# Kernel tuning notes

Measured on AMD Instinct MI355X. Metric: run time of the kernel, lower is better.

Reference implementation:

```python
import jax, jax.numpy as jnp
import numpy as np

N = 500000      # examples = M * (nr+1)
K = 20          # context set size (indices[:, 3:])
NR = 24         # negatives per positive
H = 128         # hidden_channels == node feature dim
NODES = 10000   # ingredient vocabulary


def setup_inputs() -> dict:
    key = jax.random.key(0)
    ks = jax.random.split(key, 6)
    indices = jax.random.randint(ks[0], (N, 3 + K), 0, NODES)
    x = jax.random.normal(ks[1], (NODES, H), dtype=jnp.float32)
    scale = 0.02
    W1 = jax.random.normal(ks[2], (H, 3 * H), dtype=jnp.float32) * scale
    b1 = jnp.zeros((H,), jnp.float32)
    W2 = jax.random.normal(ks[3], (H // 2, H), dtype=jnp.float32) * scale
    b2 = jnp.zeros((H // 2,), jnp.float32)
    W3 = jax.random.normal(ks[4], (1, H // 2), dtype=jnp.float32) * scale
    b3 = jnp.zeros((1,), jnp.float32)
    return {"indices": indices, "nr": NR, "x": x,
            "W1": W1, "b1": b1, "W2": W2, "b2": b2, "W3": W3, "b3": b3}


def _embed_context(ctx_idx, x, nr):
    # ctx_idx: [N, K]; one context row per group of (nr+1) examples
    new_idx = ctx_idx[:-1:nr + 1]                 # [M, K]
    emb = x[new_idx]                               # [M, K, H] gather
    s = emb.sum(axis=1)                            # [M, H]
    norm = jnp.maximum((new_idx > 0).sum(axis=1), 1).astype(x.dtype)[:, None]
    mean = s / norm                                # masked mean over context
    return jnp.repeat(mean, nr + 1, axis=0)        # broadcast back to [N, H]


def reference(indices, nr, x, W1, b1, W2, b2, W3, b3):
    ing1 = x[indices[:, 0]]                        # [N, H]
    ing2 = x[indices[:, 1]]                        # [N, H]
    set_emb = _embed_context(indices[:, 3:], x, nr)  # [N, H]
    y = jnp.concatenate([ing1, ing2, set_emb], axis=1)  # [N, 3H]
    y = jax.nn.relu(y @ W1.T + b1)
    y = jax.nn.relu(y @ W2.T + b2)
    return y @ W3.T + b3                           # [N, 1]
```

## Files before the change

kernel.cpp:

```cpp
#include <hip/hip_runtime.h>
#include <hip/hip_bf16.h>

#define N_ROWS   500000
#define NR1      25
#define NGROUPS  20000
#define KCTX     20
#define H        128
#define NODES    10000
#define IDX_COLS 23

typedef __attribute__((ext_vector_type(8))) short short8;
typedef __attribute__((ext_vector_type(4))) float f32x4;

__device__ __forceinline__ unsigned pkbf(float lo, float hi) {
  __hip_bfloat162 h = __float22bfloat162_rn(make_float2(lo, hi));
  union { __hip_bfloat162 h; unsigned u; } c; c.h = h;
  return c.u;
}
__device__ __forceinline__ float lo2f(unsigned u) {
  union { unsigned u; float f; } c; c.u = u << 16; return c.f;
}
__device__ __forceinline__ float hi2f(unsigned u) {
  union { unsigned u; float f; } c; c.u = u & 0xffff0000u; return c.f;
}

#define PN 64
#define PBLK      ((NODES + PN - 1) / PN)
#define B_PG_END  ((NGROUPS + 63) / 64)
#define B_P12     B_PG_END
#define B_IDXP    (B_P12 + 4 * PBLK)
#define B_W2FP    (B_IDXP + PBLK)
#define PRE_BLOCKS (B_W2FP + 1)

__global__ __launch_bounds__(256) void k_pre(
    const int* __restrict__ indices, const float* __restrict__ x,
    const float* __restrict__ W1, const float* __restrict__ b1,
    const float* __restrict__ W2,
    unsigned short* __restrict__ Pb, unsigned short* __restrict__ Pgb,
    unsigned short* __restrict__ w2f, int2* __restrict__ idx2) {
  __shared__ __align__(16) short lds_all[24576];

  const int tid = threadIdx.x;
  const int bid = blockIdx.x;
  const int lane = tid & 63;
  const int wvid = tid >> 6;
  const int col  = lane & 15;
  const int quad = lane >> 4;

  if (bid >= B_IDXP) {
    if (bid == B_W2FP) {
#pragma unroll
      for (int i = 0; i < 4; ++i) {
        const int fi = i * 4 + wvid;
        const int kt = fi >> 2, ct = fi & 3;
        const float* __restrict__ src =
            W2 + (size_t)(ct * 16 + col) * H + kt * 32 + quad * 8;
        const float4 v0 = *(const float4*)src;
        const float4 v1 = *(const float4*)(src + 4);
        union { short8 v; unsigned u[4]; } pk;
        pk.u[0] = pkbf(v0.x, v0.y);
        pk.u[1] = pkbf(v0.z, v0.w);
        pk.u[2] = pkbf(v1.x, v1.y);
        pk.u[3] = pkbf(v1.z, v1.w);
        *(short8*)(w2f + (size_t)(fi * 64 + lane) * 8) = pk.v;
      }
    } else {
      const int stride = PBLK * 256;
      for (int r = (bid - B_IDXP) * 256 + tid; r < N_ROWS; r += stride)
        idx2[r] = make_int2(indices[(size_t)r * IDX_COLS + 0],
                            indices[(size_t)r * IDX_COLS + 1]);
    }
    return;
  }

  if (bid < B_PG_END) {
    short* w13  = lds_all;
    short* mlds = lds_all + 16384;
    const int gbase = bid * 64;

#pragma unroll
    for (int it = 0; it < 16; ++it) {
      const int f  = it * 256 + tid;
      const int j  = f >> 5;
      const int q4 = f & 31;
      const float4 v = *(const float4*)(W1 + (size_t)j * (3 * H) + 2 * H + q4 * 4);
      const int sidx = j * 128 + (((q4 >> 1) ^ (j & 7)) << 3) + (q4 & 1) * 4;
      *(unsigned*)&w13[sidx]     = pkbf(v.x, v.y);
      *(unsigned*)&w13[sidx + 2] = pkbf(v.z, v.w);
    }

    const int jj = lane * 2;
#pragma unroll
    for (int it = 0; it < 8; ++it) {
      const int ga = gbase + wvid * 16 + it;
      const int gb = ga + 8;
      const int gac = (ga < NGROUPS) ? ga : (NGROUPS - 1);
      const int gbc = (gb < NGROUPS) ? gb : (NGROUPS - 1);
      const int* __restrict__ ra = indices + (size_t)gac * NR1 * IDX_COLS + 3;
      const int* __restrict__ rb = indices + (size_t)gbc * NR1 * IDX_COLS + 3;
      float a0 = 0.f, a1 = 0.f, c0 = 0.f, c1 = 0.f;
      int ca = 0, cb = 0;
#pragma unroll
      for (int c = 0; c < KCTX; ++c) {
        const int ia = ra[c], ib = rb[c];
        const float2 va = *(const float2*)(x + (size_t)ia * H + jj);
        const float2 vb = *(const float2*)(x + (size_t)ib * H + jj);
        a0 += va.x; a1 += va.y; c0 += vb.x; c1 += vb.y;
        ca += (ia > 0) ? 1 : 0; cb += (ib > 0) ? 1 : 0;
      }
      const float rna = 1.f / (float)((ca > 1) ? ca : 1);
      const float rnb = 1.f / (float)((cb > 1) ? cb : 1);
      {
        const int row = wvid * 16 + it;
        const int sb = row * 128 + (((lane >> 2) ^ (row & 7)) << 3) + (lane & 3) * 2;
        *(unsigned*)&mlds[sb] = pkbf(a0 * rna, a1 * rna);
      }
      {
        const int row = wvid * 16 + it + 8;
        const int sb = row * 128 + (((lane >> 2) ^ (row & 7)) << 3) + (lane & 3) * 2;
        *(unsigned*)&mlds[sb] = pkbf(c0 * rnb, c1 * rnb);
      }
    }
    __syncthreads();

    short8 Af[4];
    const int arow = wvid * 16 + col;
#pragma unroll
    for (int kt = 0; kt < 4; ++kt)
      Af[kt] = *(const short8*)
          &mlds[arow * 128 + (((kt * 4 + quad) ^ (arow & 7)) << 3)];

    f32x4 acc[8];
#pragma unroll
    for (int ct = 0; ct < 8; ++ct) acc[ct] = (f32x4)(0.f);
#pragma unroll
    for (int kt = 0; kt < 4; ++kt) {
#pragma unroll
      for (int ct = 0; ct < 8; ++ct) {
        const int brow = ct * 16 + col;
        const short8 Bf = *(const short8*)
            &w13[brow * 128 + (((kt * 4 + quad) ^ (brow & 7)) << 3)];
        acc[ct] = __builtin_amdgcn_mfma_f32_16x16x32_bf16(Af[kt], Bf, acc[ct], 0, 0, 0);
      }
    }
    float b1v[8];
#pragma unroll
    for (int ct = 0; ct < 8; ++ct) b1v[ct] = b1[ct * 16 + col];
#pragma unroll
    for (int reg = 0; reg < 4; ++reg) {
      const int g2 = gbase + wvid * 16 + quad * 4 + reg;
      if (g2 < NGROUPS) {
#pragma unroll
        for (int ct = 0; ct < 8; ++ct) {
          union { unsigned u; unsigned short s[2]; } c;
          c.u = pkbf(acc[ct][reg] + b1v[ct], 0.f);
          Pgb[(size_t)g2 * H + ct * 16 + col] = c.s[0];
        }
      }
    }
    return;
  }

  {
    short* wlds = lds_all;
    const int local = bid - B_P12;
    const int m   = local / (2 * PBLK);
    const int sub = local - m * (2 * PBLK);
    const int tbase = (sub >> 1) * PN;
    const int ch    = sub & 1;

#pragma unroll
    for (int it = 0; it < 8; ++it) {
      const int f  = it * 256 + tid;
      const int j  = f >> 5;
      const int q4 = f & 31;
      const float4 v =
          *(const float4*)(W1 + (size_t)(ch * 64 + j) * (3 * H) + m * H + q4 * 4);
      const int sidx = j * 128 + (((q4 >> 1) ^ (j & 7)) << 3) + (q4 & 1) * 4;
      *(unsigned*)&wlds[sidx]     = pkbf(v.x, v.y);
      *(unsigned*)&wlds[sidx + 2] = pkbf(v.z, v.w);
    }
    __syncthreads();

    int node = tbase + wvid * 16 + col;
    if (node > NODES - 1) node = NODES - 1;
    const float4* __restrict__ xr = (const float4*)(x + (size_t)node * H);
    short8 Af[4];
#pragma unroll
    for (int kt = 0; kt < 4; ++kt) {
      const int f4 = kt * 8 + quad * 2;
      const float4 v0 = xr[f4], v1 = xr[f4 + 1];
      union { short8 v; unsigned u[4]; } pk;
      pk.u[0] = pkbf(v0.x, v0.y);
      pk.u[1] = pkbf(v0.z, v0.w);
      pk.u[2] = pkbf(v1.x, v1.y);
      pk.u[3] = pkbf(v1.z, v1.w);
      Af[kt] = pk.v;
    }

    f32x4 acc[4];
#pragma unroll
    for (int ct = 0; ct < 4; ++ct) acc[ct] = (f32x4)(0.f);
#pragma unroll
    for (int kt = 0; kt < 4; ++kt) {
#pragma unroll
      for (int ct = 0; ct < 4; ++ct) {
        const int brow = ct * 16 + col;
        const short8 Bf = *(const short8*)
            &wlds[brow * 128 + (((kt * 4 + quad) ^ (brow & 7)) << 3)];
        acc[ct] = __builtin_amdgcn_mfma_f32_16x16x32_bf16(Af[kt], Bf, acc[ct], 0, 0, 0);
      }
    }

    unsigned short* __restrict__ Pm = Pb + (size_t)m * NODES * H;
#pragma unroll
    for (int reg = 0; reg < 4; ++reg) {
      const int n = tbase + wvid * 16 + quad * 4 + reg;
      if (n < NODES) {
#pragma unroll
        for (int ct = 0; ct < 4; ++ct) {
          union { unsigned u; unsigned short s[2]; } c;
          c.u = pkbf(acc[ct][reg], 0.f);
          Pm[(size_t)n * H + ch * 64 + ct * 16 + col] = c.s[0];
        }
      }
    }
  }
}

#define RPW 32
__global__ __launch_bounds__(256, 4) void k_main(
    const int2* __restrict__ idx2,
    const unsigned short* __restrict__ P1b, const unsigned short* __restrict__ P2b,
    const unsigned short* __restrict__ Pgb, const unsigned short* __restrict__ w2f,
    const float* __restrict__ b2, const float* __restrict__ W3,
    const float* __restrict__ b3, float* __restrict__ out) {
  __shared__ __align__(16) short w2s[16 * 64 * 8];

  const int tid  = threadIdx.x;
  const int lane = tid & 63;
  const int wv   = tid >> 6;
  const int col  = lane & 15;
  const int quad = lane >> 4;

  {
    const short8* __restrict__ src = (const short8*)w2f;
    short8* dst = (short8*)w2s;
#pragma unroll
    for (int i = 0; i < 4; ++i) dst[i * 256 + tid] = src[i * 256 + tid];
  }
  __syncthreads();

  const int Rw = (blockIdx.x * 4 + wv) * RPW;
  const int r0 = Rw + col, r1 = Rw + 16 + col;
  const int rc0 = (r0 < N_ROWS) ? r0 : (N_ROWS - 1);
  const int rc1 = (r1 < N_ROWS) ? r1 : (N_ROWS - 1);
  const int g0 = rc0 / NR1, g1 = rc1 / NR1;

  const short8* __restrict__ pc0 = (const short8*)(Pgb + (size_t)g0 * H);
  const short8* __restrict__ pc1 = (const short8*)(Pgb + (size_t)g1 * H);
  short8 uc0[4], uc1[4];
#pragma unroll
  for (int kt = 0; kt < 4; ++kt) {
    uc0[kt] = pc0[kt * 4 + quad];
    uc1[kt] = pc1[kt * 4 + quad];
  }

  const int2 iA = idx2[rc0];
  const int2 iB = idx2[rc1];

  const short8* __restrict__ pa0 = (const short8*)(P1b + (size_t)iA.x * H);
  const short8* __restrict__ pb0 = (const short8*)(P2b + (size_t)iA.y * H);
  const short8* __restrict__ pa1 = (const short8*)(P1b + (size_t)iB.x * H);
  const short8* __restrict__ pb1 = (const short8*)(P2b + (size_t)iB.y * H);
  short8 ua0[4], ub0[4], ua1[4], ub1[4];
#pragma unroll
  for (int kt = 0; kt < 4; ++kt) {
    ua0[kt] = pa0[kt * 4 + quad];
    ub0[kt] = pb0[kt * 4 + quad];
    ua1[kt] = pa1[kt * 4 + quad];
    ub1[kt] = pb1[kt * 4 + quad];
  }
  __builtin_amdgcn_sched_barrier(0);

  float b2v[4], w3v[4];
#pragma unroll
  for (int ct = 0; ct < 4; ++ct) {
    b2v[ct] = b2[ct * 16 + col];
    w3v[ct] = W3[ct * 16 + col];
  }
  const float bias3 = b3[0];

  short8 A0[4], A1[4];
#pragma unroll
  for (int kt = 0; kt < 4; ++kt) {
    union { short8 v; unsigned u[4]; } va, vb, vc;
    va.v = ua0[kt]; vb.v = ub0[kt]; vc.v = uc0[kt];
    union { short8 v; unsigned u[4]; } pk;
#pragma unroll
    for (int w = 0; w < 4; ++w) {
      const float hl = fmaxf(lo2f(va.u[w]) + lo2f(vb.u[w]) + lo2f(vc.u[w]), 0.f);
      const float hh = fmaxf(hi2f(va.u[w]) + hi2f(vb.u[w]) + hi2f(vc.u[w]), 0.f);
      pk.u[w] = pkbf(hl, hh);
    }
    A0[kt] = pk.v;
  }
#pragma unroll
  for (int kt = 0; kt < 4; ++kt) {
    union { short8 v; unsigned u[4]; } va, vb, vc;
    va.v = ua1[kt]; vb.v = ub1[kt]; vc.v = uc1[kt];
    union { short8 v; unsigned u[4]; } pk;
#pragma unroll
    for (int w = 0; w < 4; ++w) {
      const float hl = fmaxf(lo2f(va.u[w]) + lo2f(vb.u[w]) + lo2f(vc.u[w]), 0.f);
      const float hh = fmaxf(hi2f(va.u[w]) + hi2f(vb.u[w]) + hi2f(vc.u[w]), 0.f);
      pk.u[w] = pkbf(hl, hh);
    }
    A1[kt] = pk.v;
  }

  f32x4 acc0[4], acc1[4];
#pragma unroll
  for (int ct = 0; ct < 4; ++ct) { acc0[ct] = (f32x4)(0.f); acc1[ct] = (f32x4)(0.f); }
#pragma unroll
  for (int kt = 0; kt < 4; ++kt) {
#pragma unroll
    for (int ct = 0; ct < 4; ++ct) {
      const short8 Bf = *(const short8*)&w2s[((kt * 4 + ct) * 64 + lane) * 8];
      acc0[ct] = __builtin_amdgcn_mfma_f32_16x16x32_bf16(A0[kt], Bf, acc0[ct], 0, 0, 0);
      acc1[ct] = __builtin_amdgcn_mfma_f32_16x16x32_bf16(A1[kt], Bf, acc1[ct], 0, 0, 0);
    }
  }

#pragma unroll
  for (int grp = 0; grp < 2; ++grp) {
#pragma unroll
    for (int reg = 0; reg < 4; ++reg) {
      float s = 0.f;
#pragma unroll
      for (int ct = 0; ct < 4; ++ct) {
        const float a = (grp == 0) ? acc0[ct][reg] : acc1[ct][reg];
        s += fmaxf(a + b2v[ct], 0.f) * w3v[ct];
      }
      s += __shfl_xor(s, 1);
      s += __shfl_xor(s, 2);
      s += __shfl_xor(s, 4);
      s += __shfl_xor(s, 8);
      if (col == 0) {
        const int row = Rw + grp * 16 + quad * 4 + reg;
        if (row < N_ROWS) out[row] = s + bias3;
      }
    }
  }
}

extern "C" void kernel_launch(void* const* d_in, const int* in_sizes, int n_in,
                              void* d_out, int out_size, void* d_ws, size_t ws_size,
                              hipStream_t stream) {
  const int*   indices = (const int*)  d_in[0];
  const float* x  = (const float*)d_in[2];
  const float* W1 = (const float*)d_in[3];
  const float* b1 = (const float*)d_in[4];
  const float* W2 = (const float*)d_in[5];
  const float* b2 = (const float*)d_in[6];
  const float* W3 = (const float*)d_in[7];
  const float* b3 = (const float*)d_in[8];
  float* out = (float*)d_out;

  unsigned short* Pb  = (unsigned short*)d_ws;
  unsigned short* P1b = Pb;
  unsigned short* P2b = Pb + (size_t)NODES * H;
  unsigned short* Pgb = Pb + (size_t)2 * NODES * H;
  unsigned short* w2f = Pgb + (size_t)NGROUPS * H;
  int2* idx2 = (int2*)(w2f + 16 * 64 * 8);

  k_pre<<<PRE_BLOCKS, 256, 0, stream>>>(indices, x, W1, b1, W2,
                                        Pb, Pgb, w2f, idx2);
  k_main<<<(N_ROWS + 4 * RPW - 1) / (4 * RPW), 256, 0, stream>>>(
      idx2, P1b, P2b, Pgb, w2f, b2, W3, b3, out);
}
```

Measured before the change: 164.6 us.

## Stage index extraction through LDS and halve shared memory in precompute kernel

The index-pair extraction now gives each block a contiguous tile of 256 rows. The block copies that tile into LDS with coalesced int4 loads and then picks out columns 0 and 1, instead of each thread doing strided 4-byte loads from global memory. The group-mean blocks now load the W1 context slice in two 64-row halves, reusing one half-size LDS buffer. This cuts the kernel's LDS footprint from 48KB to 32KB, which should allow more resident blocks. In exchange there are extra barriers, a second W1 load phase, and many more index-extraction blocks.

```diff
diff --git a/kernel.cpp b/kernel.cpp
--- a/kernel.cpp
+++ b/kernel.cpp
@@ -26,10 +26,12 @@
 
 #define PN 64
 #define PBLK      ((NODES + PN - 1) / PN)
-#define B_PG_END  ((NGROUPS + 63) / 64)
-#define B_P12     B_PG_END
-#define B_IDXP    (B_P12 + 4 * PBLK)
-#define B_W2FP    (B_IDXP + PBLK)
+#define B_FAT     ((NGROUPS + 63) / 64)
+#define B_P12     B_FAT
+#define B_IDX     (B_P12 + 4 * PBLK)
+#define IDX_ROWS  256
+#define IDX_BLKS  ((N_ROWS + IDX_ROWS - 1) / IDX_ROWS)
+#define B_W2FP    (B_IDX + IDX_BLKS)
 #define PRE_BLOCKS (B_W2FP + 1)
 
 __global__ __launch_bounds__(256) void k_pre(
@@ -38,7 +40,7 @@
     const float* __restrict__ W2,
     unsigned short* __restrict__ Pb, unsigned short* __restrict__ Pgb,
     unsigned short* __restrict__ w2f, int2* __restrict__ idx2) {
-  __shared__ __align__(16) short lds_all[24576];
+  __shared__ __align__(16) short lds_all[16384];
 
   const int tid = threadIdx.x;
   const int bid = blockIdx.x;
@@ -47,7 +49,7 @@
   const int col  = lane & 15;
   const int quad = lane >> 4;
 
-  if (bid >= B_IDXP) {
+  if (bid >= B_IDX) {
     if (bid == B_W2FP) {
 #pragma unroll
       for (int i = 0; i < 4; ++i) {
@@ -64,30 +66,27 @@
         pk.u[3] = pkbf(v1.z, v1.w);
         *(short8*)(w2f + (size_t)(fi * 64 + lane) * 8) = pk.v;
       }
-    } else {
-      const int stride = PBLK * 256;
-      for (int r = (bid - B_IDXP) * 256 + tid; r < N_ROWS; r += stride)
-        idx2[r] = make_int2(indices[(size_t)r * IDX_COLS + 0],
-                            indices[(size_t)r * IDX_COLS + 1]);
-    }
+      return;
+    }
+    int* ilds = (int*)lds_all;
+    const int rbase = (bid - B_IDX) * IDX_ROWS;
+    const int nrows = (N_ROWS - rbase < IDX_ROWS) ? (N_ROWS - rbase) : IDX_ROWS;
+    const int nints = nrows * IDX_COLS;
+    const int* __restrict__ src = indices + (size_t)rbase * IDX_COLS;
+    const int n4 = nints >> 2;
+    const int4* __restrict__ src4 = (const int4*)src;
+    for (int i = tid; i < n4; i += 256) ((int4*)ilds)[i] = src4[i];
+    for (int i = (n4 << 2) + tid; i < nints; i += 256) ilds[i] = src[i];
+    __syncthreads();
+    for (int r = tid; r < nrows; r += 256)
+      idx2[rbase + r] = make_int2(ilds[r * IDX_COLS], ilds[r * IDX_COLS + 1]);
     return;
   }
 
-  if (bid < B_PG_END) {
-    short* w13  = lds_all;
-    short* mlds = lds_all + 16384;
+  if (bid < B_FAT) {
+    short* w13h = lds_all;
+    short* mlds = lds_all + 8192;
     const int gbase = bid * 64;
-
-#pragma unroll
-    for (int it = 0; it < 16; ++it) {
-      const int f  = it * 256 + tid;
-      const int j  = f >> 5;
-      const int q4 = f & 31;
-      const float4 v = *(const float4*)(W1 + (size_t)j * (3 * H) + 2 * H + q4 * 4);
-      const int sidx = j * 128 + (((q4 >> 1) ^ (j & 7)) << 3) + (q4 & 1) * 4;
-      *(unsigned*)&w13[sidx]     = pkbf(v.x, v.y);
-      *(unsigned*)&w13[sidx + 2] = pkbf(v.z, v.w);
-    }
 
     const int jj = lane * 2;
 #pragma unroll
@@ -121,6 +120,17 @@
         *(unsigned*)&mlds[sb] = pkbf(c0 * rnb, c1 * rnb);
       }
     }
+
+#pragma unroll
+    for (int it = 0; it < 8; ++it) {
+      const int f  = it * 256 + tid;
+      const int j  = f >> 5;
+      const int q4 = f & 31;
+      const float4 v = *(const float4*)(W1 + (size_t)j * (3 * H) + 2 * H + q4 * 4);
+      const int sidx = j * 128 + (((q4 >> 1) ^ (j & 7)) << 3) + (q4 & 1) * 4;
+      *(unsigned*)&w13h[sidx]     = pkbf(v.x, v.y);
+      *(unsigned*)&w13h[sidx + 2] = pkbf(v.z, v.w);
+    }
     __syncthreads();
 
     short8 Af[4];
@@ -130,31 +140,48 @@
       Af[kt] = *(const short8*)
           &mlds[arow * 128 + (((kt * 4 + quad) ^ (arow & 7)) << 3)];
 
-    f32x4 acc[8];
-#pragma unroll
-    for (int ct = 0; ct < 8; ++ct) acc[ct] = (f32x4)(0.f);
-#pragma unroll
-    for (int kt = 0; kt < 4; ++kt) {
-#pragma unroll
-      for (int ct = 0; ct < 8; ++ct) {
-        const int brow = ct * 16 + col;
-        const short8 Bf = *(const short8*)
-            &w13[brow * 128 + (((kt * 4 + quad) ^ (brow & 7)) << 3)];
-        acc[ct] = __builtin_amdgcn_mfma_f32_16x16x32_bf16(Af[kt], Bf, acc[ct], 0, 0, 0);
-      }
-    }
-    float b1v[8];
-#pragma unroll
-    for (int ct = 0; ct < 8; ++ct) b1v[ct] = b1[ct * 16 + col];
-#pragma unroll
-    for (int reg = 0; reg < 4; ++reg) {
-      const int g2 = gbase + wvid * 16 + quad * 4 + reg;
-      if (g2 < NGROUPS) {
-#pragma unroll
-        for (int ct = 0; ct < 8; ++ct) {
-          union { unsigned u; unsigned short s[2]; } c;
-          c.u = pkbf(acc[ct][reg] + b1v[ct], 0.f);
-          Pgb[(size_t)g2 * H + ct * 16 + col] = c.s[0];
+    for (int ch = 0; ch < 2; ++ch) {
+      if (ch == 1) {
+        __syncthreads();
+#pragma unroll
+        for (int it = 0; it < 8; ++it) {
+          const int f  = it * 256 + tid;
+          const int j  = f >> 5;
+          const int q4 = f & 31;
+          const float4 v =
+              *(const float4*)(W1 + (size_t)(64 + j) * (3 * H) + 2 * H + q4 * 4);
+          const int sidx = j * 128 + (((q4 >> 1) ^ (j & 7)) << 3) + (q4 & 1) * 4;
+          *(unsigned*)&w13h[sidx]     = pkbf(v.x, v.y);
+          *(unsigned*)&w13h[sidx + 2] = pkbf(v.z, v.w);
+        }
+        __syncthreads();
+      }
+      f32x4 acc[4];
+#pragma unroll
+      for (int ct = 0; ct < 4; ++ct) acc[ct] = (f32x4)(0.f);
+#pragma unroll
+      for (int kt = 0; kt < 4; ++kt) {
+#pragma unroll
+        for (int ct = 0; ct < 4; ++ct) {
+          const int brow = ct * 16 + col;
+          const short8 Bf = *(const short8*)
+              &w13h[brow * 128 + (((kt * 4 + quad) ^ (brow & 7)) << 3)];
+          acc[ct] = __builtin_amdgcn_mfma_f32_16x16x32_bf16(Af[kt], Bf, acc[ct], 0, 0, 0);
+        }
+      }
+      float b1v[4];
+#pragma unroll
+      for (int ct = 0; ct < 4; ++ct) b1v[ct] = b1[ch * 64 + ct * 16 + col];
+#pragma unroll
+      for (int reg = 0; reg < 4; ++reg) {
+        const int g2 = gbase + wvid * 16 + quad * 4 + reg;
+        if (g2 < NGROUPS) {
+#pragma unroll
+          for (int ct = 0; ct < 4; ++ct) {
+            union { unsigned u; unsigned short s[2]; } cc;
+            cc.u = pkbf(acc[ct][reg] + b1v[ct], 0.f);
+            Pgb[(size_t)g2 * H + ch * 64 + ct * 16 + col] = cc.s[0];
+          }
         }
       }
     }
```

Result: no change. 165.4 us (+0.5%).
